# Kernel tuning notes

Measured on AMD Instinct MI355X. Metric: run time of the kernel, lower is better.

The kernel has to match this reference:

```python
import jax, jax.numpy as jnp
import numpy as np

B, CIN, N = 4, 128, 4096
CKEY, COUT = 64, 128

def setup_inputs() -> dict:
    key = jax.random.key(0)
    k1, k2, k3, k4 = jax.random.split(key, 4)
    x = jax.random.normal(k1, (B, CIN, N), dtype=jnp.float32)
    # Conv1d(kernel_size=1, bias=False) weights as [out, in] matrices
    Wq = jax.random.normal(k2, (CKEY, CIN), dtype=jnp.float32) * (1.0 / np.sqrt(CIN))
    Wk = jax.random.normal(k3, (CKEY, CIN), dtype=jnp.float32) * (1.0 / np.sqrt(CIN))
    Wv = jax.random.normal(k4, (COUT, CIN), dtype=jnp.float32) * (1.0 / np.sqrt(CIN))
    return {"x": x, "Wq": Wq, "Wk": Wk, "Wv": Wv}

def reference(x, Wq, Wk, Wv):
    # 1x1 conv projections: [B, C, N] -> [B, C', N]
    Q = jnp.einsum('ki,bin->bkn', Wq, x)   # [B, CKEY, N]
    K = jnp.einsum('ki,bin->bkn', Wk, x)   # [B, CKEY, N]
    V = jnp.einsum('oi,bin->bon', Wv, x)   # [B, COUT, N]
    # A = softmax(Q^T K) over last dim -- NOTE: no 1/sqrt(d) scaling, as in original
    scores = jnp.einsum('bkn,bkm->bnm', Q, K)     # [B, N, N]
    A = jax.nn.softmax(scores, axis=2)
    # out = (A @ V^T)^T -> [B, COUT, N]
    out = jnp.einsum('bnm,bom->bon', A, V)
    return out
```

## Files before the change

kernel.cpp:

```cpp
#include <hip/hip_runtime.h>
#include <hip/hip_bf16.h>

#define NN    4096
#define BB    4
#define CIN_  128
#define COUT_ 128

typedef __attribute__((ext_vector_type(8))) short bf16x8;
typedef __attribute__((ext_vector_type(4))) short bf16x4;
typedef __attribute__((ext_vector_type(4))) float f32x4;
typedef __attribute__((ext_vector_type(2))) int   i32x2;

#define MFMA16 __builtin_amdgcn_mfma_f32_16x16x32_bf16
#define SWK(row, g) ((((row) << 6)) + ((((g) ^ ((row) & 7))) << 3))

__device__ __forceinline__ float bf2f(short s) {
    union { unsigned int u; float f; } c; c.u = ((unsigned int)(unsigned short)s) << 16; return c.f;
}
__device__ __forceinline__ short f2bf(float f) {
    union { float f; unsigned int u; } c; c.f = f;
    unsigned int r = c.u + 0x7fffu + ((c.u >> 16) & 1u);
    return (short)(r >> 16);
}
__device__ __forceinline__ float fexp2(float x) {
#if __has_builtin(__builtin_amdgcn_exp2f)
    return __builtin_amdgcn_exp2f(x);
#else
    return exp2f(x);
#endif
}
__device__ __forceinline__ unsigned int pack_bf16(float a, float b) {
    union { float f; unsigned int u; } ca, cb; ca.f = a; cb.f = b;
    unsigned int ua = ca.u + 0x8000u, ub = cb.u + 0x8000u;
#if __has_builtin(__builtin_amdgcn_perm)
    return __builtin_amdgcn_perm(ub, ua, 0x07060302u);
#else
    return (ua >> 16) | (ub & 0xffff0000u);
#endif
}

__global__ __launch_bounds__(256) void proj_kernel(const float* __restrict__ x,
                                                   const float* __restrict__ Wq,
                                                   const float* __restrict__ Wk,
                                                   const float* __restrict__ Wv,
                                                   short* __restrict__ Qh, short* __restrict__ Ql,
                                                   short* __restrict__ Kh, short* __restrict__ Kl,
                                                   short* __restrict__ Vb) {
    __shared__ __align__(16) short xsh[16 * 64 * 8];
    __shared__ __align__(16) short xsl[16 * 64 * 8];

    int tid  = threadIdx.x;
    int b    = blockIdx.y;
    int gz   = blockIdx.z;
    int gn0  = blockIdx.x * 64;
    int wave = tid >> 6;
    int lane = tid & 63;
    int quad = lane >> 4;
    int l15  = lane & 15;

    const float* xb = x + (size_t)b * CIN_ * NN + gn0;
#pragma unroll
    for (int rep = 0; rep < 4; ++rep) {
        int slot = rep * 256 + tid;
        int c = slot >> 6, n = slot & 63;
        bf16x8 h8, l8;
#pragma unroll
        for (int j = 0; j < 8; ++j) {
            float f = xb[(c * 8 + j) * NN + n];
            short h = f2bf(f);
            h8[j] = h;
            l8[j] = f2bf(f - bf2f(h));
        }
        *(bf16x8*)(xsh + (c * 64 + n) * 8) = h8;
        *(bf16x8*)(xsl + (c * 64 + n) * 8) = l8;
    }
    __syncthreads();

    int rg = gz * 4 + wave;

    const float* wrow;
    float scale = 1.0f;
    if (rg < 4)      { wrow = Wq + (rg * 16 + l15) * CIN_; scale = 1.4426950408889634f; }
    else if (rg < 8) { wrow = Wk + ((rg - 4) * 16 + l15) * CIN_; }
    else             { wrow = Wv + ((rg - 8) * 16 + l15) * CIN_; }

    bf16x8 wh[4], wl[4];
#pragma unroll
    for (int kc = 0; kc < 4; ++kc) {
        const float* wp = wrow + kc * 32 + quad * 8;
#pragma unroll
        for (int j = 0; j < 8; ++j) {
            float w = wp[j] * scale;
            short h = f2bf(w);
            wh[kc][j] = h;
            wl[kc][j] = f2bf(w - bf2f(h));
        }
    }

    f32x4 acc[4];
#pragma unroll
    for (int ct = 0; ct < 4; ++ct) acc[ct] = (f32x4){0.f, 0.f, 0.f, 0.f};

#pragma unroll
    for (int kc = 0; kc < 4; ++kc) {
#pragma unroll
        for (int ct = 0; ct < 4; ++ct) {
            bf16x8 xh = *(const bf16x8*)(xsh + (((kc * 4 + quad) * 64) + ct * 16 + l15) * 8);
            bf16x8 xl = *(const bf16x8*)(xsl + (((kc * 4 + quad) * 64) + ct * 16 + l15) * 8);
            acc[ct] = MFMA16(wh[kc], xh, acc[ct], 0, 0, 0);
            acc[ct] = MFMA16(wh[kc], xl, acc[ct], 0, 0, 0);
            acc[ct] = MFMA16(wl[kc], xh, acc[ct], 0, 0, 0);
        }
    }

    if (rg < 8) {
        short* H = (rg < 4) ? Qh : Kh;
        short* L = (rg < 4) ? Ql : Kl;
        int rb    = (rg < 4) ? rg : (rg - 4);
        int chunk = rb * 2 + (quad >> 1);
        int sub   = (quad & 1) * 4;
#pragma unroll
        for (int ct = 0; ct < 4; ++ct) {
            int n = gn0 + ct * 16 + l15;
            bf16x4 h4, l4;
#pragma unroll
            for (int r = 0; r < 4; ++r) {
                float f = acc[ct][r];
                short h = f2bf(f);
                h4[r] = h;
                l4[r] = f2bf(f - bf2f(h));
            }
            *(bf16x4*)(H + (((b * 8 + chunk) * NN) + n) * 8 + sub) = h4;
            *(bf16x4*)(L + (((b * 8 + chunk) * NN) + n) * 8 + sub) = l4;
        }
    } else {
        int o0 = rg * 16 + quad * 4 - 128;
#pragma unroll
        for (int ct = 0; ct < 4; ++ct) {
            int n = gn0 + ct * 16 + l15;
#pragma unroll
            for (int r = 0; r < 4; ++r)
                Vb[((size_t)(b * COUT_ + o0 + r)) * NN + n] = f2bf(acc[ct][r]);
        }
    }
}

__global__ __launch_bounds__(256, 2) void flash_kernel(const short* __restrict__ Qh,
                                                       const short* __restrict__ Ql,
                                                       const short* __restrict__ Kh,
                                                       const short* __restrict__ Kl,
                                                       const short* __restrict__ Vb,
                                                       float* __restrict__ outp,
                                                       float* __restrict__ lsum,
                                                       int S, int direct) {
    __shared__ __align__(16) short VT[128 * 64];
    __shared__ __align__(16) short PW[4 * 32 * 64];

    int tid  = threadIdx.x;
    int bx   = blockIdx.x;
    int b    = bx / S;
    int s    = bx - b * S;
    int qt   = blockIdx.y;
    int wave = tid >> 6;
    int lane = tid & 63;
    int quad = lane >> 4;
    int l15  = lane & 15;

    int nq0 = qt * 128 + wave * 32 + l15;
    bf16x8 qh0[2], qh1[2], ql0[2], ql1[2];
#pragma unroll
    for (int u = 0; u < 2; ++u) {
        int nq = nq0 + u * 16;
        qh0[u] = *(const bf16x8*)(Qh + (((b * 8 + quad)     * NN) + nq) * 8);
        qh1[u] = *(const bf16x8*)(Qh + (((b * 8 + 4 + quad) * NN) + nq) * 8);
        ql0[u] = *(const bf16x8*)(Ql + (((b * 8 + quad)     * NN) + nq) * 8);
        ql1[u] = *(const bf16x8*)(Ql + (((b * 8 + 4 + quad) * NN) + nq) * 8);
    }

    f32x4 O[2][8];
#pragma unroll
    for (int u = 0; u < 2; ++u)
#pragma unroll
        for (int f = 0; f < 8; ++f) O[u][f] = (f32x4){0.f, 0.f, 0.f, 0.f};
    float lp[2] = {0.f, 0.f};

    int vrow = tid & 127, vc0 = (tid >> 7) * 4;
    short* pwb = PW + wave * 2048;

    int KPS   = NN / S;
    int kb    = s * KPS;
    int iters = KPS / 64;

    const short* KhB = Kh + (size_t)b * 8 * NN * 8;
    const short* KlB = Kl + (size_t)b * 8 * NN * 8;
    const short* VbB = Vb + (size_t)b * COUT_ * NN;

    bf16x8 nv[4];
#pragma unroll
    for (int q = 0; q < 4; ++q)
        nv[q] = *(const bf16x8*)(VbB + (size_t)vrow * NN + kb + (vc0 + q) * 8);

    for (int it = 0; it < iters; ++it) {
        bf16x8 kh0[4], kh1[4], kl0[4], kl1[4];
#pragma unroll
        for (int f = 0; f < 4; ++f) {
            int row = kb + f * 16 + l15;
            kh0[f] = *(const bf16x8*)(KhB + ((quad       * NN) + row) * 8);
            kh1[f] = *(const bf16x8*)(KhB + (((4 + quad) * NN) + row) * 8);
            kl0[f] = *(const bf16x8*)(KlB + ((quad       * NN) + row) * 8);
            kl1[f] = *(const bf16x8*)(KlB + (((4 + quad) * NN) + row) * 8);
        }

#pragma unroll
        for (int q = 0; q < 4; ++q)
            *(bf16x8*)(VT + SWK(vrow, vc0 + q)) = nv[q];
        __syncthreads();

        if (it + 1 < iters) {
            int nb = kb + 64;
#pragma unroll
            for (int q = 0; q < 4; ++q)
                nv[q] = *(const bf16x8*)(VbB + (size_t)vrow * NN + nb + (vc0 + q) * 8);
        }

        f32x4 sA[2][4];
#pragma unroll
        for (int f = 0; f < 4; ++f) {
#pragma unroll
            for (int u = 0; u < 2; ++u) {
                f32x4 acc = (f32x4){0.f, 0.f, 0.f, 0.f};
                acc = MFMA16(kh0[f], qh0[u], acc, 0, 0, 0);
                acc = MFMA16(kh1[f], qh1[u], acc, 0, 0, 0);
                acc = MFMA16(kl0[f], qh0[u], acc, 0, 0, 0);
                acc = MFMA16(kl1[f], qh1[u], acc, 0, 0, 0);
                acc = MFMA16(kh0[f], ql0[u], acc, 0, 0, 0);
                acc = MFMA16(kh1[f], ql1[u], acc, 0, 0, 0);
                sA[u][f] = acc;
            }
        }

#pragma unroll
        for (int u = 0; u < 2; ++u) {
            int row = u * 16 + l15;
#pragma unroll
            for (int f = 0; f < 4; ++f) {
                float p0 = fexp2(sA[u][f][0]);
                float p1 = fexp2(sA[u][f][1]);
                float p2 = fexp2(sA[u][f][2]);
                float p3 = fexp2(sA[u][f][3]);
                lp[u] += (p0 + p1) + (p2 + p3);
                unsigned int w0 = pack_bf16(p0, p1);
                unsigned int w1 = pack_bf16(p2, p3);
                *(i32x2*)(pwb + SWK(row, f * 2 + (quad >> 1)) + (quad & 1) * 4) =
                    (i32x2){(int)w0, (int)w1};
            }
        }

#pragma unroll
        for (int g = 0; g < 2; ++g) {
            bf16x8 pb0 = *(const bf16x8*)(pwb + SWK(l15,      g * 4 + quad));
            bf16x8 pb1 = *(const bf16x8*)(pwb + SWK(16 + l15, g * 4 + quad));
#pragma unroll
            for (int f8 = 0; f8 < 8; ++f8) {
                bf16x8 vA = *(const bf16x8*)(VT + SWK(f8 * 16 + l15, g * 4 + quad));
                O[0][f8] = MFMA16(vA, pb0, O[0][f8], 0, 0, 0);
                O[1][f8] = MFMA16(vA, pb1, O[1][f8], 0, 0, 0);
            }
        }
        __syncthreads();
        kb += 64;
    }

#pragma unroll
    for (int u = 0; u < 2; ++u) {
        lp[u] += __shfl_xor(lp[u], 16, 64);
        lp[u] += __shfl_xor(lp[u], 32, 64);
    }

#pragma unroll
    for (int u = 0; u < 2; ++u) {
        int n = nq0 + u * 16;
        if (direct) {
            float inv = 1.f / lp[u];
#pragma unroll
            for (int f8 = 0; f8 < 8; ++f8)
#pragma unroll
                for (int r = 0; r < 4; ++r) {
                    int o = f8 * 16 + quad * 4 + r;
                    outp[((size_t)(b * COUT_ + o)) * NN + n] = O[u][f8][r] * inv;
                }
        } else {
#pragma unroll
            for (int f8 = 0; f8 < 8; ++f8)
#pragma unroll
                for (int r = 0; r < 4; ++r) {
                    int o = f8 * 16 + quad * 4 + r;
                    outp[((size_t)((b * S + s) * COUT_ + o)) * NN + n] = O[u][f8][r];
                }
            if (quad == 0) lsum[(b * S + s) * NN + n] = lp[u];
        }
    }
}

__global__ __launch_bounds__(256, 4) void merge_kernel(const float* __restrict__ Opart,
                                                       const float* __restrict__ lsum,
                                                       float* __restrict__ out, int S) {
    int idx = blockIdx.x * 256 + threadIdx.x;
    int n0  = (idx & (NN / 4 - 1)) * 4;
    int rest = idx >> 10;
    int o = rest & (COUT_ - 1);
    int b = rest >> 7;

    f32x4 den = (f32x4){0.f, 0.f, 0.f, 0.f};
    f32x4 acc = (f32x4){0.f, 0.f, 0.f, 0.f};
    for (int s = 0; s < S; ++s) {
        f32x4 l  = *(const f32x4*)(lsum + (b * S + s) * NN + n0);
        f32x4 ov = *(const f32x4*)(Opart + ((size_t)((b * S + s) * COUT_ + o)) * NN + n0);
#pragma unroll
        for (int j = 0; j < 4; ++j) {
            den[j] += l[j];
            acc[j] += ov[j];
        }
    }
    f32x4 res;
#pragma unroll
    for (int j = 0; j < 4; ++j) res[j] = acc[j] / den[j];
    *(f32x4*)(out + ((size_t)(b * COUT_ + o)) * NN + n0) = res;
}

extern "C" void kernel_launch(void* const* d_in, const int* in_sizes, int n_in,
                              void* d_out, int out_size, void* d_ws, size_t ws_size,
                              hipStream_t stream) {
    const float* x  = (const float*)d_in[0];
    const float* Wq = (const float*)d_in[1];
    const float* Wk = (const float*)d_in[2];
    const float* Wv = (const float*)d_in[3];

    char* ws = (char*)d_ws;
    short* Qh = (short*)ws;
    short* Ql = Qh + 1048576;
    short* Kh = Ql + 1048576;
    short* Kl = Kh + 1048576;
    short* Vb = Kl + 1048576;
    size_t base = 4ull * 2097152 + 4194304;
    const size_t MLSZ  = (size_t)BB * NN * 4;
    const size_t OPART = 8388608;

    int S;
    if      (ws_size >= base + 4 * (MLSZ + OPART)) S = 4;
    else if (ws_size >= base + 2 * (MLSZ + OPART)) S = 2;
    else                                           S = 1;
    int direct = (S == 1);

    float* lsum  = (float*)(ws + base);
    float* Opart = (float*)(ws + base + (size_t)S * MLSZ);

    proj_kernel<<<dim3(NN / 64, BB, 4), 256, 0, stream>>>(x, Wq, Wk, Wv, Qh, Ql, Kh, Kl, Vb);
    flash_kernel<<<dim3(BB * S, NN / 128), 256, 0, stream>>>(
        Qh, Ql, Kh, Kl, Vb, direct ? (float*)d_out : Opart, lsum, S, direct);
    if (!direct)
        merge_kernel<<<BB * COUT_ * NN / 4 / 256, 256, 0, stream>>>(Opart, lsum, (float*)d_out, S);
}
```

Baseline: 124.0 us.

## Double-buffer V tile in LDS, prefetch next K tile, add MFMA priority hints

Doubles the V tile in shared memory so the next V tile is written while the current one is consumed, which removes one barrier per iteration. V global loads now run two tiles ahead. The K fragments for the next iteration are loaded into registers right after the QK MFMAs, so their latency overlaps the softmax and PV work. s_setprio is raised around the MFMA blocks. The cost is twice the LDS for V, which can lower occupancy, plus more register pressure from holding prefetched K.

Result: no change. 126.2 us (+1.7%).

```diff
diff --git a/kernel.cpp b/kernel.cpp
--- a/kernel.cpp
+++ b/kernel.cpp
@@ -153,7 +153,7 @@
                                                        float* __restrict__ outp,
                                                        float* __restrict__ lsum,
                                                        int S, int direct) {
-    __shared__ __align__(16) short VT[128 * 64];
+    __shared__ __align__(16) short VT[2 * 128 * 64];
     __shared__ __align__(16) short PW[4 * 32 * 64];
 
     int tid  = threadIdx.x;
@@ -199,31 +199,42 @@
 #pragma unroll
     for (int q = 0; q < 4; ++q)
         nv[q] = *(const bf16x8*)(VbB + (size_t)vrow * NN + kb + (vc0 + q) * 8);
-
+#pragma unroll
+    for (int q = 0; q < 4; ++q)
+        *(bf16x8*)(VT + SWK(vrow, vc0 + q)) = nv[q];
+    if (iters > 1) {
+#pragma unroll
+        for (int q = 0; q < 4; ++q)
+            nv[q] = *(const bf16x8*)(VbB + (size_t)vrow * NN + kb + 64 + (vc0 + q) * 8);
+    }
+    bf16x8 kh0[4], kh1[4], kl0[4], kl1[4];
+#pragma unroll
+    for (int f = 0; f < 4; ++f) {
+        int row = kb + f * 16 + l15;
+        kh0[f] = *(const bf16x8*)(KhB + ((quad       * NN) + row) * 8);
+        kh1[f] = *(const bf16x8*)(KhB + (((4 + quad) * NN) + row) * 8);
+        kl0[f] = *(const bf16x8*)(KlB + ((quad       * NN) + row) * 8);
+        kl1[f] = *(const bf16x8*)(KlB + (((4 + quad) * NN) + row) * 8);
+    }
+    __syncthreads();
+
+    int cur = 0;
     for (int it = 0; it < iters; ++it) {
-        bf16x8 kh0[4], kh1[4], kl0[4], kl1[4];
-#pragma unroll
-        for (int f = 0; f < 4; ++f) {
-            int row = kb + f * 16 + l15;
-            kh0[f] = *(const bf16x8*)(KhB + ((quad       * NN) + row) * 8);
-            kh1[f] = *(const bf16x8*)(KhB + (((4 + quad) * NN) + row) * 8);
-            kl0[f] = *(const bf16x8*)(KlB + ((quad       * NN) + row) * 8);
-            kl1[f] = *(const bf16x8*)(KlB + (((4 + quad) * NN) + row) * 8);
-        }
-
-#pragma unroll
-        for (int q = 0; q < 4; ++q)
-            *(bf16x8*)(VT + SWK(vrow, vc0 + q)) = nv[q];
-        __syncthreads();
-
         if (it + 1 < iters) {
-            int nb = kb + 64;
+            short* vt1 = VT + ((cur ^ 1) << 13);
+#pragma unroll
+            for (int q = 0; q < 4; ++q)
+                *(bf16x8*)(vt1 + SWK(vrow, vc0 + q)) = nv[q];
+        }
+        if (it + 2 < iters) {
+            int nb = kb + 128;
 #pragma unroll
             for (int q = 0; q < 4; ++q)
                 nv[q] = *(const bf16x8*)(VbB + (size_t)vrow * NN + nb + (vc0 + q) * 8);
         }
 
         f32x4 sA[2][4];
+        __builtin_amdgcn_s_setprio(1);
 #pragma unroll
         for (int f = 0; f < 4; ++f) {
 #pragma unroll
@@ -236,6 +247,19 @@
                 acc = MFMA16(kh0[f], ql0[u], acc, 0, 0, 0);
                 acc = MFMA16(kh1[f], ql1[u], acc, 0, 0, 0);
                 sA[u][f] = acc;
+            }
+        }
+        __builtin_amdgcn_s_setprio(0);
+
+        if (it + 1 < iters) {
+            int kn = kb + 64;
+#pragma unroll
+            for (int f = 0; f < 4; ++f) {
+                int row = kn + f * 16 + l15;
+                kh0[f] = *(const bf16x8*)(KhB + ((quad       * NN) + row) * 8);
+                kh1[f] = *(const bf16x8*)(KhB + (((4 + quad) * NN) + row) * 8);
+                kl0[f] = *(const bf16x8*)(KlB + ((quad       * NN) + row) * 8);
+                kl1[f] = *(const bf16x8*)(KlB + (((4 + quad) * NN) + row) * 8);
             }
         }
 
@@ -256,18 +280,25 @@
             }
         }
 
-#pragma unroll
-        for (int g = 0; g < 2; ++g) {
-            bf16x8 pb0 = *(const bf16x8*)(pwb + SWK(l15,      g * 4 + quad));
-            bf16x8 pb1 = *(const bf16x8*)(pwb + SWK(16 + l15, g * 4 + quad));
-#pragma unroll
-            for (int f8 = 0; f8 < 8; ++f8) {
-                bf16x8 vA = *(const bf16x8*)(VT + SWK(f8 * 16 + l15, g * 4 + quad));
-                O[0][f8] = MFMA16(vA, pb0, O[0][f8], 0, 0, 0);
-                O[1][f8] = MFMA16(vA, pb1, O[1][f8], 0, 0, 0);
-            }
-        }
+        {
+            const short* vt = VT + (cur << 13);
+            __builtin_amdgcn_s_setprio(1);
+#pragma unroll
+            for (int g = 0; g < 2; ++g) {
+                bf16x8 pb0 = *(const bf16x8*)(pwb + SWK(l15,      g * 4 + quad));
+                bf16x8 pb1 = *(const bf16x8*)(pwb + SWK(16 + l15, g * 4 + quad));
+#pragma unroll
+                for (int f8 = 0; f8 < 8; ++f8) {
+                    bf16x8 vA = *(const bf16x8*)(vt + SWK(f8 * 16 + l15, g * 4 + quad));
+                    O[0][f8] = MFMA16(vA, pb0, O[0][f8], 0, 0, 0);
+                    O[1][f8] = MFMA16(vA, pb1, O[1][f8], 0, 0, 0);
+                }
+            }
+            __builtin_amdgcn_s_setprio(0);
+        }
+
         __syncthreads();
+        cur ^= 1;
         kb += 64;
     }
 
```
